# Performance work log

Hardware: AMD Instinct MI355X
Metric: run time of the kernel (lower is better)

## Reference

```python
import jax, jax.numpy as jnp
import numpy as np
from jax import lax

NMS_THRESH = 0.7  # opt.rpn_nms_thresh
N_BOXES = 8192


def setup_inputs() -> dict:
    key = jax.random.key(0)
    k1, k2, k3, k4, k5 = jax.random.split(key, 5)
    H, W = 1024, 1536
    # realistic word-box proposals on a document page (cxcywh)
    cx = jax.random.uniform(k1, (N_BOXES,)) * W
    cy = jax.random.uniform(k2, (N_BOXES,)) * H
    w = jax.random.uniform(k3, (N_BOXES,)) * 300.0 + 10.0
    h = jax.random.uniform(k4, (N_BOXES,)) * 80.0 + 8.0
    rpn_boxes = jnp.stack([cx, cy, w, h], axis=-1)[None]  # (1, N, 4)
    rpn_scores = jax.random.normal(k5, (1, N_BOXES, 1), dtype=jnp.float32)
    return {
        "rpn_boxes": rpn_boxes.astype(jnp.float32),
        "rpn_scores": rpn_scores,
        "img_h": H,
        "img_w": W,
        "num_proposals": 1000,
    }


def _iou_matrix(b):
    # b: (N, 4) xyxy -> (N, N) pairwise IoU
    area = (b[:, 2] - b[:, 0]) * (b[:, 3] - b[:, 1])
    x1 = jnp.maximum(b[:, None, 0], b[None, :, 0])
    y1 = jnp.maximum(b[:, None, 1], b[None, :, 1])
    x2 = jnp.minimum(b[:, None, 2], b[None, :, 2])
    y2 = jnp.minimum(b[:, None, 3], b[None, :, 3])
    inter = jnp.clip(x2 - x1, 0.0) * jnp.clip(y2 - y1, 0.0)
    union = area[:, None] + area[None, :] - inter
    return inter / jnp.maximum(union, 1e-8)


def _greedy_nms_keep(iou, valid):
    # sequential greedy NMS over score-sorted boxes; keep[i] True if not
    # suppressed by any earlier kept box with IoU > thresh
    n = iou.shape[0]
    idxs = jnp.arange(n)

    def body(i, keep):
        sup = jnp.any(keep & (iou[i] > NMS_THRESH) & (idxs < i))
        return keep.at[i].set(keep[i] & ~sup)

    return lax.fori_loop(0, n, body, valid)


def _localization_test(rpn_boxes, rpn_scores, img_h, img_w, num_proposals):
    boxes = rpn_boxes[0]          # (N, 4) cxcywh
    scores = rpn_scores[0, :, 0]  # (N,)
    cx, cy, w, h = boxes[:, 0], boxes[:, 1], boxes[:, 2], boxes[:, 3]
    # clip to image bounds (box_utils.clip_boxes, 'cxcywh')
    x_max, y_max = float(img_w - 1), float(img_h - 1)
    x1 = jnp.clip(cx - 0.5 * w, 0.0, x_max)
    x2 = jnp.clip(cx + 0.5 * w, 0.0, x_max)
    y1 = jnp.clip(cy - 0.5 * h, 0.0, y_max)
    y2 = jnp.clip(cy + 0.5 * h, 0.0, y_max)
    cw, ch = x2 - x1, y2 - y1
    cxcywh = jnp.stack([0.5 * (x1 + x2), 0.5 * (y1 + y2), cw, ch], axis=-1)
    xyxy = jnp.stack([x1, y1, x2, y2], axis=-1)
    valid = (cw > 0.0) & (ch > 0.0)
    probs = jax.nn.sigmoid(scores)
    masked_probs = jnp.where(valid, probs, -jnp.inf)
    # sort by score descending (torchvision.ops.nms order)
    order = jnp.argsort(-masked_probs)
    xyxy_s = xyxy[order]
    cxcywh_s = cxcywh[order]
    probs_s = masked_probs[order]
    valid_s = valid[order]
    iou = _iou_matrix(xyxy_s)
    keep = _greedy_nms_keep(iou, valid_s)
    kept_scores = jnp.where(keep, probs_s, -jnp.inf)
    vals, top_idx = lax.top_k(kept_scores, num_proposals)
    out = cxcywh_s[top_idx]                          # (M, 4) cxcywh
    out = jnp.where(jnp.isfinite(vals)[:, None], out, 0.0)  # zero-pad if < M kept
    return out


def reference(rpn_boxes, rpn_scores, img_h, img_w, num_proposals):
    return _localization_test(rpn_boxes, rpn_scores, img_h, img_w, num_proposals)
```

## Files before the change

kernel.cpp:

```cpp
#include <hip/hip_runtime.h>

#define NBOX 8192

__global__ void prep_kernel(const float4* __restrict__ boxes,
                            const float* __restrict__ scores,
                            const int* __restrict__ ph, const int* __restrict__ pw,
                            unsigned long long* __restrict__ keys,
                            float4* __restrict__ xyxy, float4* __restrict__ cxcywh,
                            unsigned char* __restrict__ validb,
                            int* __restrict__ rank,
                            float4* __restrict__ out, int npro,
                            int* __restrict__ counter) {
#pragma clang fp contract(off)
    int i = blockIdx.x * blockDim.x + threadIdx.x;
    if (i == 0) *counter = 0;
    if (i >= NBOX) return;
    if (i < npro) out[i] = make_float4(0.f, 0.f, 0.f, 0.f);
    rank[i] = 0;
    float xmax = (float)(*pw - 1);
    float ymax = (float)(*ph - 1);
    float4 b = boxes[i];
    float hw = 0.5f * b.z;
    float hh = 0.5f * b.w;
    float x1 = fminf(fmaxf(b.x - hw, 0.0f), xmax);
    float x2 = fminf(fmaxf(b.x + hw, 0.0f), xmax);
    float y1 = fminf(fmaxf(b.y - hh, 0.0f), ymax);
    float y2 = fminf(fmaxf(b.y + hh, 0.0f), ymax);
    float cw = x2 - x1, chh = y2 - y1;
    bool valid = (cw > 0.0f) && (chh > 0.0f);
    xyxy[i]   = make_float4(x1, y1, x2, y2);
    cxcywh[i] = make_float4(0.5f * (x1 + x2), 0.5f * (y1 + y2), cw, chh);
    validb[i] = valid ? 1 : 0;
    float s = scores[i];
    unsigned int sb  = __float_as_uint(s);
    unsigned int asc = (sb & 0x80000000u) ? ~sb : (sb | 0x80000000u);
    unsigned int hi  = valid ? ~asc : 0xFFFFFFFFu;
    keys[i] = ((unsigned long long)hi << 32) | (unsigned int)i;
}

__global__ __launch_bounds__(256)
void edge_kernel(const float4* __restrict__ xyxy,
                 const unsigned long long* __restrict__ keys,
                 unsigned int* __restrict__ edges, int* __restrict__ counter,
                 int ecap) {
#pragma clang fp contract(off)
    __shared__ float4 tj[128];
    __shared__ float  ta[128];
    __shared__ unsigned long long tk[128];
    int b = blockIdx.x;
    int bi = (int)((sqrtf(8.0f * (float)b + 1.0f) - 1.0f) * 0.5f);
    while ((bi + 1) * (bi + 2) / 2 <= b) ++bi;
    while (bi * (bi + 1) / 2 > b) --bi;
    int bj = b - bi * (bi + 1) / 2;
    int t = threadIdx.x;
    int ib = bi * 128, jb = bj * 128;
    if (t < 128) {
        float4 v = xyxy[jb + t];
        tj[t] = v;
        ta[t] = (v.z - v.x) * (v.w - v.y);
        tk[t] = keys[jb + t];
    }
    __syncthreads();
    int r = t >> 1, l = t & 1;
    int i = ib + r;
    float4 b4 = xyxy[i];
    float ai = (b4.z - b4.x) * (b4.w - b4.y);
    unsigned long long ki = keys[i];
    for (int jj = l; jj < 128; jj += 2) {
        int j = jb + jj;
        if (j >= i) break;
        float4 bj4 = tj[jj];
        float ix1 = fmaxf(b4.x, bj4.x);
        float iy1 = fmaxf(b4.y, bj4.y);
        float ix2 = fminf(b4.z, bj4.z);
        float iy2 = fminf(b4.w, bj4.w);
        float iw  = fmaxf(ix2 - ix1, 0.0f);
        float ih  = fmaxf(iy2 - iy1, 0.0f);
        float inter = iw * ih;
        float uni   = ai + ta[jj] - inter;
        float iou   = inter / fmaxf(uni, 1e-8f);
        if (iou > 0.7f) {
            unsigned long long kj = tk[jj];
            unsigned int loser, winner;
            if (ki < kj) { winner = (unsigned int)i; loser = (unsigned int)j; }
            else         { winner = (unsigned int)j; loser = (unsigned int)i; }
            int pos = atomicAdd(counter, 1);
            if (pos < ecap) edges[pos] = (loser << 16) | winner;
        }
    }
}

__global__ __launch_bounds__(1024)
void resolve_kernel(const unsigned char* __restrict__ validg,
                    const unsigned int* __restrict__ edges,
                    const int* __restrict__ counter,
                    const unsigned long long* __restrict__ keys,
                    unsigned char* __restrict__ keptg,
                    unsigned long long* __restrict__ rkeys, int ecap) {
    __shared__ unsigned char kept[NBOX];
    __shared__ unsigned char validb[NBOX];
    __shared__ unsigned char sup[NBOX];
    __shared__ int s_changed;
    int t = threadIdx.x;
    int E = *counter;
    if (E > ecap) E = ecap;
    for (int i = t; i < NBOX; i += 1024) {
        unsigned char v = validg[i];
        validb[i] = v;
        kept[i] = v;
    }
    __syncthreads();
    for (int iter = 0; iter < NBOX; ++iter) {
        for (int i = t; i < NBOX; i += 1024) sup[i] = 0;
        if (t == 0) s_changed = 0;
        __syncthreads();
        for (int e = t; e < E; e += 1024) {
            unsigned int ed = edges[e];
            int l = (int)(ed >> 16), w = (int)(ed & 0xFFFFu);
            if (kept[w]) sup[l] = 1;
        }
        __syncthreads();
        int changed = 0;
        for (int i = t; i < NBOX; i += 1024) {
            unsigned char nk = (unsigned char)(validb[i] && !sup[i]);
            if (nk != kept[i]) { kept[i] = nk; changed = 1; }
        }
        if (changed) s_changed = 1;
        __syncthreads();
        int done = (s_changed == 0);
        __syncthreads();
        if (done) break;
    }
    for (int i = t; i < NBOX; i += 1024) {
        unsigned char k = kept[i];
        keptg[i] = k;
        rkeys[i] = k ? keys[i] : ~0ull;
    }
}

#define RCHUNK 1024
__global__ __launch_bounds__(256)
void rank_partial_kernel(const unsigned long long* __restrict__ keys,
                         const unsigned long long* __restrict__ rkeys,
                         int* __restrict__ rank) {
    __shared__ unsigned long long tk[RCHUNK];
    int t = threadIdx.x;
    int chunk = blockIdx.x >> 8;
    int rowg  = blockIdx.x & 255;
    int jbase = chunk * RCHUNK;
#pragma unroll
    for (int m = 0; m < RCHUNK / 256; ++m) tk[t + m * 256] = rkeys[jbase + t + m * 256];
    __syncthreads();
    int row = rowg * 32 + (t >> 3);
    int lane = t & 7;
    unsigned long long ki = keys[row];
    int partial = 0;
#pragma unroll 16
    for (int j = lane; j < RCHUNK; j += 8) partial += (tk[j] < ki) ? 1 : 0;
    partial += __shfl_down(partial, 4, 8);
    partial += __shfl_down(partial, 2, 8);
    partial += __shfl_down(partial, 1, 8);
    if (lane == 0 && partial) atomicAdd(&rank[row], partial);
}

__global__ void scatter_kernel(const unsigned char* __restrict__ keptg,
                               const int* __restrict__ rank,
                               const float4* __restrict__ cxcywh,
                               float4* __restrict__ out, int npro) {
    int i = blockIdx.x * blockDim.x + threadIdx.x;
    if (i >= NBOX) return;
    if (keptg[i]) {
        int r = rank[i];
        if (r < npro) out[r] = cxcywh[i];
    }
}

extern "C" void kernel_launch(void* const* d_in, const int* in_sizes, int n_in,
                              void* d_out, int out_size, void* d_ws, size_t ws_size,
                              hipStream_t stream) {
    const float4* boxes  = (const float4*)d_in[0];
    const float* scores  = (const float*)d_in[1];
    const int* ph        = (const int*)d_in[2];
    const int* pw        = (const int*)d_in[3];

    char* ws = (char*)d_ws;
    size_t off = 0;
    unsigned long long* keys  = (unsigned long long*)(ws + off); off += (size_t)NBOX * 8;
    unsigned long long* rkeys = (unsigned long long*)(ws + off); off += (size_t)NBOX * 8;
    float4* xyxy     = (float4*)(ws + off); off += (size_t)NBOX * 16;
    float4* cxcywh   = (float4*)(ws + off); off += (size_t)NBOX * 16;
    int* rank        = (int*)(ws + off);    off += (size_t)NBOX * 4;
    unsigned char* validb = (unsigned char*)(ws + off); off += NBOX;
    unsigned char* keptg  = (unsigned char*)(ws + off); off += NBOX;
    off = (off + 63) & ~(size_t)63;
    int* counter = (int*)(ws + off); off += 64;
    unsigned int* edges = (unsigned int*)(ws + off);

    int ecap = 262144;
    if (ws_size > off) {
        size_t room = (ws_size - off) / 4;
        if ((size_t)ecap > room) ecap = (int)room;
    } else {
        ecap = 0;
    }
    int npro = out_size / 4;

    prep_kernel<<<NBOX / 256, 256, 0, stream>>>(boxes, scores, ph, pw, keys, xyxy,
                                                cxcywh, validb, rank,
                                                (float4*)d_out, npro, counter);
    int ntiles = NBOX / 128;
    edge_kernel<<<ntiles * (ntiles + 1) / 2, 256, 0, stream>>>(xyxy, keys, edges,
                                                               counter, ecap);
    resolve_kernel<<<1, 1024, 0, stream>>>(validb, edges, counter, keys, keptg,
                                           rkeys, ecap);
    rank_partial_kernel<<<(NBOX / 32) * (NBOX / RCHUNK), 256, 0, stream>>>(keys, rkeys, rank);
    scatter_kernel<<<NBOX / 256, 256, 0, stream>>>(keptg, rank, cxcywh,
                                                   (float4*)d_out, npro);
}
```

Measured before the change: 64.15 us.

## Fuse prep into edge kernel, bitpack resolve state, fuse rank with scatter

The separate prep kernel is removed: the edge kernel now recomputes clipped boxes and sort keys on the fly, and diagonal tiles write the per-box outputs and initialize rank, done counters and output padding. The resolve kernel keeps its kept, valid and suppressed flags as 32-bit bitmasks updated with atomicOr instead of byte arrays. The rank kernel takes over the scatter step through a last-block-done counter per row group. The aim is fewer launches and less shared-memory traffic, at the cost of redundant box math in every edge tile and an extra memset launch.

```diff
diff --git a/kernel.cpp b/kernel.cpp
--- a/kernel.cpp
+++ b/kernel.cpp
@@ -2,45 +2,15 @@
 
 #define NBOX 8192
 
-__global__ void prep_kernel(const float4* __restrict__ boxes,
-                            const float* __restrict__ scores,
-                            const int* __restrict__ ph, const int* __restrict__ pw,
-                            unsigned long long* __restrict__ keys,
-                            float4* __restrict__ xyxy, float4* __restrict__ cxcywh,
-                            unsigned char* __restrict__ validb,
-                            int* __restrict__ rank,
-                            float4* __restrict__ out, int npro,
-                            int* __restrict__ counter) {
-#pragma clang fp contract(off)
-    int i = blockIdx.x * blockDim.x + threadIdx.x;
-    if (i == 0) *counter = 0;
-    if (i >= NBOX) return;
-    if (i < npro) out[i] = make_float4(0.f, 0.f, 0.f, 0.f);
-    rank[i] = 0;
-    float xmax = (float)(*pw - 1);
-    float ymax = (float)(*ph - 1);
-    float4 b = boxes[i];
-    float hw = 0.5f * b.z;
-    float hh = 0.5f * b.w;
-    float x1 = fminf(fmaxf(b.x - hw, 0.0f), xmax);
-    float x2 = fminf(fmaxf(b.x + hw, 0.0f), xmax);
-    float y1 = fminf(fmaxf(b.y - hh, 0.0f), ymax);
-    float y2 = fminf(fmaxf(b.y + hh, 0.0f), ymax);
-    float cw = x2 - x1, chh = y2 - y1;
-    bool valid = (cw > 0.0f) && (chh > 0.0f);
-    xyxy[i]   = make_float4(x1, y1, x2, y2);
-    cxcywh[i] = make_float4(0.5f * (x1 + x2), 0.5f * (y1 + y2), cw, chh);
-    validb[i] = valid ? 1 : 0;
-    float s = scores[i];
-    unsigned int sb  = __float_as_uint(s);
-    unsigned int asc = (sb & 0x80000000u) ? ~sb : (sb | 0x80000000u);
-    unsigned int hi  = valid ? ~asc : 0xFFFFFFFFu;
-    keys[i] = ((unsigned long long)hi << 32) | (unsigned int)i;
-}
-
 __global__ __launch_bounds__(256)
-void edge_kernel(const float4* __restrict__ xyxy,
-                 const unsigned long long* __restrict__ keys,
+void edge_kernel(const float4* __restrict__ boxes,
+                 const float* __restrict__ scores,
+                 const int* __restrict__ ph, const int* __restrict__ pw,
+                 unsigned long long* __restrict__ keys_g,
+                 unsigned char* __restrict__ validb_g,
+                 float4* __restrict__ cxcywh_g,
+                 float4* __restrict__ out, int npro,
+                 int* __restrict__ rank_g, int* __restrict__ done_g,
                  unsigned int* __restrict__ edges, int* __restrict__ counter,
                  int ecap) {
 #pragma clang fp contract(off)
@@ -54,26 +24,63 @@
     int bj = b - bi * (bi + 1) / 2;
     int t = threadIdx.x;
     int ib = bi * 128, jb = bj * 128;
+    float xmax = (float)(*pw - 1);
+    float ymax = (float)(*ph - 1);
+
     if (t < 128) {
-        float4 v = xyxy[jb + t];
-        tj[t] = v;
-        ta[t] = (v.z - v.x) * (v.w - v.y);
-        tk[t] = keys[jb + t];
-    }
-    __syncthreads();
+        int j = jb + t;
+        float4 bx = boxes[j];
+        float hw = 0.5f * bx.z, hh = 0.5f * bx.w;
+        float x1 = fminf(fmaxf(bx.x - hw, 0.0f), xmax);
+        float x2 = fminf(fmaxf(bx.x + hw, 0.0f), xmax);
+        float y1 = fminf(fmaxf(bx.y - hh, 0.0f), ymax);
+        float y2 = fminf(fmaxf(bx.y + hh, 0.0f), ymax);
+        float cw = x2 - x1, ch = y2 - y1;
+        bool valid = (cw > 0.0f) && (ch > 0.0f);
+        tj[t] = make_float4(x1, y1, x2, y2);
+        ta[t] = cw * ch;
+        float s = scores[j];
+        unsigned int sb  = __float_as_uint(s);
+        unsigned int asc = (sb & 0x80000000u) ? ~sb : (sb | 0x80000000u);
+        unsigned int hi  = valid ? ~asc : 0xFFFFFFFFu;
+        tk[t] = ((unsigned long long)hi << 32) | (unsigned int)j;
+        if (bi == bj) {
+            keys_g[j]   = tk[t];
+            validb_g[j] = valid ? 1 : 0;
+            cxcywh_g[j] = make_float4(0.5f * (x1 + x2), 0.5f * (y1 + y2), cw, ch);
+        }
+    }
+    if (bj == 0) {
+        if (t < 128) rank_g[ib + t] = 0;
+        if (t < 4)   done_g[bi * 4 + t] = 0;
+        if (t < 16) { int r = bi * 16 + t; if (r < npro) out[r] = make_float4(0.f, 0.f, 0.f, 0.f); }
+    }
+    __syncthreads();
+
     int r = t >> 1, l = t & 1;
     int i = ib + r;
-    float4 b4 = xyxy[i];
-    float ai = (b4.z - b4.x) * (b4.w - b4.y);
-    unsigned long long ki = keys[i];
+    float4 bx = boxes[i];
+    float hw = 0.5f * bx.z, hh = 0.5f * bx.w;
+    float x1 = fminf(fmaxf(bx.x - hw, 0.0f), xmax);
+    float x2 = fminf(fmaxf(bx.x + hw, 0.0f), xmax);
+    float y1 = fminf(fmaxf(bx.y - hh, 0.0f), ymax);
+    float y2 = fminf(fmaxf(bx.y + hh, 0.0f), ymax);
+    float ai = (x2 - x1) * (y2 - y1);
+    float s = scores[i];
+    unsigned int sb  = __float_as_uint(s);
+    unsigned int asc = (sb & 0x80000000u) ? ~sb : (sb | 0x80000000u);
+    bool vi = ((x2 - x1) > 0.0f) && ((y2 - y1) > 0.0f);
+    unsigned int hi = vi ? ~asc : 0xFFFFFFFFu;
+    unsigned long long ki = ((unsigned long long)hi << 32) | (unsigned int)i;
+
     for (int jj = l; jj < 128; jj += 2) {
         int j = jb + jj;
         if (j >= i) break;
         float4 bj4 = tj[jj];
-        float ix1 = fmaxf(b4.x, bj4.x);
-        float iy1 = fmaxf(b4.y, bj4.y);
-        float ix2 = fminf(b4.z, bj4.z);
-        float iy2 = fminf(b4.w, bj4.w);
+        float ix1 = fmaxf(x1, bj4.x);
+        float iy1 = fmaxf(y1, bj4.y);
+        float ix2 = fminf(x2, bj4.z);
+        float iy2 = fminf(y2, bj4.w);
         float iw  = fmaxf(ix2 - ix1, 0.0f);
         float ih  = fmaxf(iy2 - iy1, 0.0f);
         float inter = iw * ih;
@@ -97,81 +104,91 @@
                     const unsigned long long* __restrict__ keys,
                     unsigned char* __restrict__ keptg,
                     unsigned long long* __restrict__ rkeys, int ecap) {
-    __shared__ unsigned char kept[NBOX];
-    __shared__ unsigned char validb[NBOX];
-    __shared__ unsigned char sup[NBOX];
+    __shared__ unsigned int keptw[256];
+    __shared__ unsigned int validw[256];
+    __shared__ unsigned int sup[256];
     __shared__ int s_changed;
     int t = threadIdx.x;
     int E = *counter;
     if (E > ecap) E = ecap;
-    for (int i = t; i < NBOX; i += 1024) {
-        unsigned char v = validg[i];
-        validb[i] = v;
-        kept[i] = v;
-    }
+    int wv = t >> 6, lane = t & 63;
+    for (int g = wv; g < 128; g += 16) {
+        unsigned long long m = __ballot(validg[g * 64 + lane] != 0);
+        if (lane == 0) {
+            validw[2 * g]     = (unsigned int)m;
+            validw[2 * g + 1] = (unsigned int)(m >> 32);
+        }
+    }
+    __syncthreads();
+    if (t < 256) keptw[t] = validw[t];
     __syncthreads();
     for (int iter = 0; iter < NBOX; ++iter) {
-        for (int i = t; i < NBOX; i += 1024) sup[i] = 0;
+        if (t < 256) sup[t] = 0u;
         if (t == 0) s_changed = 0;
         __syncthreads();
         for (int e = t; e < E; e += 1024) {
             unsigned int ed = edges[e];
-            int l = (int)(ed >> 16), w = (int)(ed & 0xFFFFu);
-            if (kept[w]) sup[l] = 1;
-        }
-        __syncthreads();
-        int changed = 0;
-        for (int i = t; i < NBOX; i += 1024) {
-            unsigned char nk = (unsigned char)(validb[i] && !sup[i]);
-            if (nk != kept[i]) { kept[i] = nk; changed = 1; }
-        }
-        if (changed) s_changed = 1;
+            unsigned int l = ed >> 16, w = ed & 0xFFFFu;
+            if ((keptw[w >> 5] >> (w & 31)) & 1u)
+                atomicOr(&sup[l >> 5], 1u << (l & 31));
+        }
+        __syncthreads();
+        if (t < 256) {
+            unsigned int nk = validw[t] & ~sup[t];
+            if (nk != keptw[t]) { keptw[t] = nk; s_changed = 1; }
+        }
         __syncthreads();
         int done = (s_changed == 0);
         __syncthreads();
         if (done) break;
     }
     for (int i = t; i < NBOX; i += 1024) {
-        unsigned char k = kept[i];
-        keptg[i] = k;
+        unsigned int k = (keptw[i >> 5] >> (i & 31)) & 1u;
+        keptg[i] = (unsigned char)k;
         rkeys[i] = k ? keys[i] : ~0ull;
     }
 }
 
 #define RCHUNK 1024
 __global__ __launch_bounds__(256)
-void rank_partial_kernel(const unsigned long long* __restrict__ keys,
+void rank_scatter_kernel(const unsigned long long* __restrict__ keys,
                          const unsigned long long* __restrict__ rkeys,
-                         int* __restrict__ rank) {
-    __shared__ unsigned long long tk[RCHUNK];
+                         const unsigned char* __restrict__ keptg,
+                         const float4* __restrict__ cxcywh,
+                         int* __restrict__ rank, int* __restrict__ done,
+                         float4* __restrict__ out, int npro) {
+    __shared__ unsigned long long tkl[RCHUNK];
+    __shared__ int s_last;
     int t = threadIdx.x;
     int chunk = blockIdx.x >> 8;
     int rowg  = blockIdx.x & 255;
     int jbase = chunk * RCHUNK;
 #pragma unroll
-    for (int m = 0; m < RCHUNK / 256; ++m) tk[t + m * 256] = rkeys[jbase + t + m * 256];
+    for (int m = 0; m < RCHUNK / 256; ++m) tkl[t + m * 256] = rkeys[jbase + t + m * 256];
     __syncthreads();
     int row = rowg * 32 + (t >> 3);
     int lane = t & 7;
     unsigned long long ki = keys[row];
     int partial = 0;
 #pragma unroll 16
-    for (int j = lane; j < RCHUNK; j += 8) partial += (tk[j] < ki) ? 1 : 0;
+    for (int j = lane; j < RCHUNK; j += 8) partial += (tkl[j] < ki) ? 1 : 0;
     partial += __shfl_down(partial, 4, 8);
     partial += __shfl_down(partial, 2, 8);
     partial += __shfl_down(partial, 1, 8);
     if (lane == 0 && partial) atomicAdd(&rank[row], partial);
-}
-
-__global__ void scatter_kernel(const unsigned char* __restrict__ keptg,
-                               const int* __restrict__ rank,
-                               const float4* __restrict__ cxcywh,
-                               float4* __restrict__ out, int npro) {
-    int i = blockIdx.x * blockDim.x + threadIdx.x;
-    if (i >= NBOX) return;
-    if (keptg[i]) {
-        int r = rank[i];
-        if (r < npro) out[r] = cxcywh[i];
+    __syncthreads();
+    if (t == 0) {
+        __threadfence();
+        int old = atomicAdd(&done[rowg], 1);
+        s_last = (old == 7) ? 1 : 0;
+    }
+    __syncthreads();
+    if (s_last && t < 32) {
+        int r2 = rowg * 32 + t;
+        if (keptg[r2]) {
+            int rk = atomicAdd(&rank[r2], 0);
+            if (rk < npro) out[rk] = cxcywh[r2];
+        }
     }
 }
 
@@ -187,9 +204,9 @@
     size_t off = 0;
     unsigned long long* keys  = (unsigned long long*)(ws + off); off += (size_t)NBOX * 8;
     unsigned long long* rkeys = (unsigned long long*)(ws + off); off += (size_t)NBOX * 8;
-    float4* xyxy     = (float4*)(ws + off); off += (size_t)NBOX * 16;
-    float4* cxcywh   = (float4*)(ws + off); off += (size_t)NBOX * 16;
-    int* rank        = (int*)(ws + off);    off += (size_t)NBOX * 4;
+    float4* cxcywh = (float4*)(ws + off); off += (size_t)NBOX * 16;
+    int* rank      = (int*)(ws + off);    off += (size_t)NBOX * 4;
+    int* done      = (int*)(ws + off);    off += 256 * 4;
     unsigned char* validb = (unsigned char*)(ws + off); off += NBOX;
     unsigned char* keptg  = (unsigned char*)(ws + off); off += NBOX;
     off = (off + 63) & ~(size_t)63;
@@ -205,15 +222,13 @@
     }
     int npro = out_size / 4;
 
-    prep_kernel<<<NBOX / 256, 256, 0, stream>>>(boxes, scores, ph, pw, keys, xyxy,
-                                                cxcywh, validb, rank,
-                                                (float4*)d_out, npro, counter);
+    hipMemsetAsync(counter, 0, 64, stream);
     int ntiles = NBOX / 128;
-    edge_kernel<<<ntiles * (ntiles + 1) / 2, 256, 0, stream>>>(xyxy, keys, edges,
-                                                               counter, ecap);
+    edge_kernel<<<ntiles * (ntiles + 1) / 2, 256, 0, stream>>>(
+        boxes, scores, ph, pw, keys, validb, cxcywh,
+        (float4*)d_out, npro, rank, done, edges, counter, ecap);
     resolve_kernel<<<1, 1024, 0, stream>>>(validb, edges, counter, keys, keptg,
                                            rkeys, ecap);
-    rank_partial_kernel<<<(NBOX / 32) * (NBOX / RCHUNK), 256, 0, stream>>>(keys, rkeys, rank);
-    scatter_kernel<<<NBOX / 256, 256, 0, stream>>>(keptg, rank, cxcywh,
-                                                   (float4*)d_out, npro);
-}
+    rank_scatter_kernel<<<(NBOX / 32) * (NBOX / RCHUNK), 256, 0, stream>>>(
+        keys, rkeys, keptg, cxcywh, rank, done, (float4*)d_out, npro);
+}
```

After: 83.66 us. 30.4% more time.
